# Optimization experiments

Measured on AMD Instinct MI355X. Metric: run time of the kernel, lower is better.

## Reference

```python
import jax, jax.numpy as jnp
import numpy as np

B, S, H, NH = 4, 1024, 1024, 16
HD = H // NH
CAUSAL_HEADS = 4
META_HEADS = NH // 4
CAUSAL_W = 0.7                      # cognitive_state['reasoning']['causal_active'] > 0.5 -> branch on
META_W = ((0.9 - 0.8) / 0.2) * 0.3  # awareness_level = 0.9 > 0.8 -> meta branch on, blend = 0.15


def _mha(xq, xkv, Win, bi, Wout, bout, nh):
    """torch nn.MultiheadAttention (batch_first) with packed in_proj [H, 3H]."""
    b, sq, h = xq.shape
    sk = xkv.shape[1]
    hd = h // nh
    q = (xq @ Win[:, :h] + bi[:h]).reshape(b, sq, nh, hd).transpose(0, 2, 1, 3)
    k = (xkv @ Win[:, h:2 * h] + bi[h:2 * h]).reshape(b, sk, nh, hd).transpose(0, 2, 1, 3)
    v = (xkv @ Win[:, 2 * h:] + bi[2 * h:]).reshape(b, sk, nh, hd).transpose(0, 2, 1, 3)
    scores = jnp.einsum('bhqd,bhkd->bhqk', q, k) / jnp.sqrt(jnp.asarray(hd, q.dtype))
    probs = jax.nn.softmax(scores, axis=-1)
    ctx = jnp.einsum('bhqk,bhkd->bhqd', probs, v)
    return ctx.transpose(0, 2, 1, 3).reshape(b, sq, h) @ Wout + bout


def _forward(hidden_states, cons_vec, Wq, bq, Wk, bk, Wv, bv, cg_W, cg_b, am_W, am_b,
             ca_Win, ca_bin, ca_Wout, ca_bout, mc_Win, mc_bin, mc_Wout, mc_bout, Wo, bo):
    b, s, h = hidden_states.shape
    q = (hidden_states @ Wq + bq).reshape(b, s, NH, HD).transpose(0, 2, 1, 3)
    k = (hidden_states @ Wk + bk).reshape(b, s, NH, HD).transpose(0, 2, 1, 3)
    v = (hidden_states @ Wv + bv).reshape(b, s, NH, HD).transpose(0, 2, 1, 3)
    scores = jnp.einsum('bhqd,bhkd->bhqk', q, k) / jnp.sqrt(jnp.asarray(HD, q.dtype))
    # consciousness-gated score modulation: sigmoid(gate(x) + awareness(cons_vec)) per (query, head)
    mod = jax.nn.sigmoid(hidden_states @ cg_W + cg_b + (cons_vec @ am_W + am_b))  # [B,S,NH]
    scores = scores * mod.transpose(0, 2, 1)[..., None]  # [B,NH,S,1] broadcast over keys
    probs = jax.nn.softmax(scores, axis=-1)
    ctx = jnp.einsum('bhqk,bhkd->bhqd', probs, v).transpose(0, 2, 1, 3).reshape(b, s, h)
    # causal MHA branch (active: causal_active=0.7 > 0.5)
    causal_ctx = _mha(hidden_states, hidden_states, ca_Win, ca_bin, ca_Wout, ca_bout, CAUSAL_HEADS)
    ctx = ctx * (1.0 - CAUSAL_W) + causal_ctx * CAUSAL_W
    # metacognitive MHA branch (active: awareness=0.9 > 0.8)
    meta_ctx = _mha(ctx, ctx, mc_Win, mc_bin, mc_Wout, mc_bout, META_HEADS)
    ctx = ctx * (1.0 - META_W) + meta_ctx * META_W
    return ctx @ Wo + bo


def setup_inputs() -> dict:
    key = jax.random.key(0)
    ks = jax.random.split(key, 16)
    sc = 0.02
    d = {
        'hidden_states': jax.random.normal(ks[0], (B, S, H), jnp.float32),
        'cons_vec': jax.random.uniform(ks[1], (16,), jnp.float32),
        'Wq': jax.random.normal(ks[2], (H, H), jnp.float32) * sc, 'bq': jnp.zeros((H,), jnp.float32),
        'Wk': jax.random.normal(ks[3], (H, H), jnp.float32) * sc, 'bk': jnp.zeros((H,), jnp.float32),
        'Wv': jax.random.normal(ks[4], (H, H), jnp.float32) * sc, 'bv': jnp.zeros((H,), jnp.float32),
        'cg_W': jax.random.normal(ks[5], (H, NH), jnp.float32) * sc, 'cg_b': jnp.zeros((NH,), jnp.float32),
        'am_W': jax.random.normal(ks[6], (16, NH), jnp.float32) * sc, 'am_b': jnp.zeros((NH,), jnp.float32),
        'ca_Win': jax.random.normal(ks[7], (H, 3 * H), jnp.float32) * sc, 'ca_bin': jnp.zeros((3 * H,), jnp.float32),
        'ca_Wout': jax.random.normal(ks[8], (H, H), jnp.float32) * sc, 'ca_bout': jnp.zeros((H,), jnp.float32),
        'mc_Win': jax.random.normal(ks[9], (H, 3 * H), jnp.float32) * sc, 'mc_bin': jnp.zeros((3 * H,), jnp.float32),
        'mc_Wout': jax.random.normal(ks[10], (H, H), jnp.float32) * sc, 'mc_bout': jnp.zeros((H,), jnp.float32),
        'Wo': jax.random.normal(ks[11], (H, H), jnp.float32) * sc, 'bo': jnp.zeros((H,), jnp.float32),
    }
    return d


def reference(hidden_states, cons_vec, Wq, bq, Wk, bk, Wv, bv, cg_W, cg_b, am_W, am_b,
              ca_Win, ca_bin, ca_Wout, ca_bout, mc_Win, mc_bin, mc_Wout, mc_bout, Wo, bo):
    return _forward(hidden_states, cons_vec, Wq, bq, Wk, bk, Wv, bv, cg_W, cg_b, am_W, am_b,
                    ca_Win, ca_bin, ca_Wout, ca_bout, mc_Win, mc_bin, mc_Wout, mc_bout, Wo, bo)
```

## Files before the change

### kernel.cpp

```cpp
#include <hip/hip_runtime.h>
#include <stdint.h>

typedef unsigned short u16;
typedef __attribute__((ext_vector_type(8))) short short8;
typedef __attribute__((ext_vector_type(4))) float f32x4;

#define MFMA16(a,b,c) __builtin_amdgcn_mfma_f32_16x16x32_bf16((a),(b),(c),0,0,0)

__device__ __forceinline__ u16 f2bf(float f) {
  union { float f; uint32_t u; } v; v.f = f;
  uint32_t r = v.u + 0x7FFFu + ((v.u >> 16) & 1u);
  return (u16)(r >> 16);
}
__device__ __forceinline__ float bf2f(uint32_t u) {
  union { uint32_t i; float f; } v; v.i = u << 16; return v.f;
}
__device__ __forceinline__ void async_copy16(void* lds, const void* g) {
  __builtin_amdgcn_global_load_lds(
      (const __attribute__((address_space(1))) uint32_t*)g,
      (__attribute__((address_space(3))) uint32_t*)lds, 16, 0, 0);
}

__device__ __forceinline__ void transpose8x8(uint32_t r[4], int lane8) {
  uint32_t a0, a1, a2, a3;
  a0 = __shfl_xor(r[0], 4); a1 = __shfl_xor(r[1], 4);
  a2 = __shfl_xor(r[2], 4); a3 = __shfl_xor(r[3], 4);
  if (lane8 & 4) { r[0] = a2; r[1] = a3; } else { r[2] = a0; r[3] = a1; }
  a0 = __shfl_xor(r[0], 2); a1 = __shfl_xor(r[1], 2);
  a2 = __shfl_xor(r[2], 2); a3 = __shfl_xor(r[3], 2);
  if (lane8 & 2) { r[0] = a1; r[2] = a3; } else { r[1] = a0; r[3] = a2; }
  a0 = __shfl_xor(r[0], 1); a1 = __shfl_xor(r[1], 1);
  a2 = __shfl_xor(r[2], 1); a3 = __shfl_xor(r[3], 1);
  uint32_t sel = (lane8 & 1) ? 0x03020706u : 0x05040100u;
  r[0] = __builtin_amdgcn_perm(a0, r[0], sel);
  r[1] = __builtin_amdgcn_perm(a1, r[1], sel);
  r[2] = __builtin_amdgcn_perm(a2, r[2], sel);
  r[3] = __builtin_amdgcn_perm(a3, r[3], sel);
}

__global__ __launch_bounds__(256) void castmod_kernel(
    const float* __restrict__ X, u16* __restrict__ Xbf,
    const float* __restrict__ cgW, const float* __restrict__ cgb,
    const float* __restrict__ cons, const float* __restrict__ amW,
    const float* __restrict__ amb, float* __restrict__ modp) {
  __shared__ float xs[1024];
  __shared__ float part[16][16];
  __shared__ float am[16];
  int row = blockIdx.x, t = threadIdx.x;
  {
    float4 v = ((const float4*)(X + (size_t)row * 1024))[t];
    xs[t * 4 + 0] = v.x; xs[t * 4 + 1] = v.y; xs[t * 4 + 2] = v.z; xs[t * 4 + 3] = v.w;
    uint2 o;
    o.x = (uint32_t)f2bf(v.x) | ((uint32_t)f2bf(v.y) << 16);
    o.y = (uint32_t)f2bf(v.z) | ((uint32_t)f2bf(v.w) << 16);
    ((uint2*)Xbf)[(size_t)row * 256 + t] = o;
  }
  if (t < 16) {
    float a = amb[t];
#pragma unroll
    for (int i = 0; i < 16; i++) a += cons[i] * amW[i * 16 + t];
    am[t] = a;
  }
  __syncthreads();
  int h = t & 15, ch = t >> 4;
  float p = 0.f;
#pragma unroll 8
  for (int k = ch * 64; k < ch * 64 + 64; k++) p += xs[k] * cgW[k * 16 + h];
  part[ch][h] = p;
  __syncthreads();
  if (t < 16) {
    float s = cgb[t] + am[t];
#pragma unroll
    for (int c = 0; c < 16; c++) s += part[c][t];
    int b = row >> 10, si = row & 1023;
    modp[((size_t)(b * 16 + t)) * 1024 + si] = 0.125f / (1.f + __expf(-s));
  }
}

struct PrepArgs {
  const float* src[12];
  u16* dst[12];
  int sstride[12];
  const float* cabin; const float* bq; const float* bk; const float* bv;
  float* biasBig; float* lbuf;
};
__global__ __launch_bounds__(256) void prep_weights(PrepArgs p) {
  int z = blockIdx.z;
  int tx = threadIdx.x & 31, ty = threadIdx.x >> 5;
  if (z < 12) {
    __shared__ float tile[32][33];
    const float* __restrict__ in = p.src[z];
    u16* __restrict__ out = p.dst[z];
    int sstr = p.sstride[z];
    int c0 = blockIdx.x * 32, r0 = blockIdx.y * 32;
#pragma unroll
    for (int j = 0; j < 4; j++)
      tile[ty + j * 8][tx] = in[(size_t)(r0 + ty + j * 8) * sstr + c0 + tx];
    __syncthreads();
#pragma unroll
    for (int j = 0; j < 4; j++)
      out[(size_t)(c0 + ty + j * 8) * 1024 + r0 + tx] = f2bf(tile[tx][ty + j * 8]);
  } else {
    int id = blockIdx.y * 32 + blockIdx.x, t = threadIdx.x;
    if (id < 24) {
      int i = id * 256 + t;
      float v;
      if (i < 3072) v = p.cabin[i];
      else if (i < 4096) v = p.bq[i - 3072];
      else if (i < 5120) v = p.bk[i - 4096];
      else v = p.bv[i - 5120];
      p.biasBig[i] = v;
    } else if (id < 152) {
      p.lbuf[(id - 24) * 256 + t] = 0.f;
    }
  }
}

template <int OUT_F32, int HAS_EXTRA, int BN>
__global__ __launch_bounds__(256, 3) void gemm_bt(
    const u16* __restrict__ A, const u16* __restrict__ Bt,
    const float* __restrict__ bias, const u16* __restrict__ extra,
    float alpha, float beta, void* __restrict__ Cout, int M, int N, int K) {
  constexpr int NJ = BN / 32;
  __shared__ u16 As[128 * 64];
  __shared__ u16 Bs[BN * 64];
  const int t = threadIdx.x;
  const int w = t >> 6, l = t & 63, lm = l & 15, lg = l >> 4;
  const int wm = w & 1, wn = w >> 1;
  const int m0 = blockIdx.y * 128, n0 = blockIdx.x * BN;
  const int rl = l >> 3, gsrc8 = ((l & 7) ^ (rl & 7)) * 8;
  const f32x4 fzero = {0.f, 0.f, 0.f, 0.f};
  f32x4 acc[4][NJ];
#pragma unroll
  for (int i = 0; i < 4; i++)
#pragma unroll
    for (int j = 0; j < NJ; j++) acc[i][j] = fzero;

  for (int kt = 0; kt < K; kt += 64) {
    __syncthreads();
#pragma unroll
    for (int c = 0; c < 4; c++) {
      int rb = c * 32 + w * 8;
      async_copy16(&As[rb * 64], A + (size_t)(m0 + rb + rl) * K + kt + gsrc8);
    }
#pragma unroll
    for (int c = 0; c < BN / 32; c++) {
      int rb = c * 32 + w * 8;
      async_copy16(&Bs[rb * 64], Bt + (size_t)(n0 + rb + rl) * K + kt + gsrc8);
    }
    __syncthreads();
#pragma unroll
    for (int kk = 0; kk < 2; kk++) {
      short8 af[4], bf[NJ];
      const int gph = ((kk * 4 + lg) ^ (lm & 7)) * 8;
#pragma unroll
      for (int i = 0; i < 4; i++)
        af[i] = *(const short8*)&As[(wm * 64 + i * 16 + lm) * 64 + gph];
#pragma unroll
      for (int j = 0; j < NJ; j++)
        bf[j] = *(const short8*)&Bs[(wn * (BN / 2) + j * 16 + lm) * 64 + gph];
#pragma unroll
      for (int i = 0; i < 4; i++)
#pragma unroll
        for (int j = 0; j < NJ; j++) acc[i][j] = MFMA16(af[i], bf[j], acc[i][j]);
    }
  }
#pragma unroll
  for (int i = 0; i < 4; i++) {
    int row0 = m0 + wm * 64 + i * 16 + lg * 4;
#pragma unroll
    for (int j = 0; j < NJ; j++) {
      int col = n0 + wn * (BN / 2) + j * 16 + lm;
      float bc = bias[col];
#pragma unroll
      for (int r = 0; r < 4; r++) {
        size_t idx = (size_t)(row0 + r) * N + col;
        float v = acc[i][j][r] + bc;
        if constexpr (HAS_EXTRA) v = alpha * v + beta * bf2f(extra[idx]);
        if constexpr (OUT_F32) ((float*)Cout)[idx] = v;
        else ((u16*)Cout)[idx] = f2bf(v);
      }
    }
  }
}

__global__ __launch_bounds__(256, 3) void gemm_in3(
    const u16* __restrict__ A, const u16* __restrict__ BtBig,
    const float* __restrict__ bias, u16* __restrict__ qkOut,
    u16* __restrict__ Vtb, u16* __restrict__ qkvm) {
  constexpr int K = 1024;
  __shared__ u16 As[128 * 64];
  __shared__ u16 Bs[128 * 64];
  const int t = threadIdx.x;
  const int w = t >> 6, l = t & 63, lm = l & 15, lg = l >> 4;
  const int wm = w & 1, wn = w >> 1;
  const int m0 = blockIdx.y * 128, n0 = blockIdx.x * 128;
  const int rl = l >> 3, gsrc8 = ((l & 7) ^ (rl & 7)) * 8;
  const f32x4 fzero = {0.f, 0.f, 0.f, 0.f};
  f32x4 acc[4][4];
#pragma unroll
  for (int i = 0; i < 4; i++)
#pragma unroll
    for (int j = 0; j < 4; j++) acc[i][j] = fzero;

  for (int kt = 0; kt < K; kt += 64) {
    __syncthreads();
#pragma unroll
    for (int c = 0; c < 4; c++) {
      int rb = c * 32 + w * 8;
      async_copy16(&As[rb * 64], A + (size_t)(m0 + rb + rl) * K + kt + gsrc8);
      async_copy16(&Bs[rb * 64], BtBig + (size_t)(n0 + rb + rl) * K + kt + gsrc8);
    }
    __syncthreads();
#pragma unroll
    for (int kk = 0; kk < 2; kk++) {
      short8 af[4], bf[4];
      const int gph = ((kk * 4 + lg) ^ (lm & 7)) * 8;
#pragma unroll
      for (int i = 0; i < 4; i++)
        af[i] = *(const short8*)&As[(wm * 64 + i * 16 + lm) * 64 + gph];
#pragma unroll
      for (int j = 0; j < 4; j++)
        bf[j] = *(const short8*)&Bs[(wn * 64 + j * 16 + lm) * 64 + gph];
#pragma unroll
      for (int i = 0; i < 4; i++)
#pragma unroll
        for (int j = 0; j < 4; j++) acc[i][j] = MFMA16(af[i], bf[j], acc[i][j]);
    }
  }
#pragma unroll
  for (int i = 0; i < 4; i++) {
    int row0 = m0 + wm * 64 + i * 16 + lg * 4;
#pragma unroll
    for (int j = 0; j < 4; j++) {
      int col = n0 + wn * 64 + j * 16 + lm;
      float bc = bias[col];
      if (col < 2048) {
#pragma unroll
        for (int r = 0; r < 4; r++)
          qkOut[(size_t)(row0 + r) * 2048 + col] = f2bf(acc[i][j][r] + bc);
      } else if (col < 3072) {
        int b = row0 >> 10, q0 = row0 & 1023;
        int z = b * 4 + ((col - 2048) >> 8), d = (col - 2048) & 255;
        union { u16 pk[4]; uint2 v; } u;
#pragma unroll
        for (int r = 0; r < 4; r++) u.pk[r] = f2bf(acc[i][j][r] + bc);
        *(uint2*)&Vtb[((size_t)z * 256 + d) * 1024 + q0] = u.v;
      } else {
#pragma unroll
        for (int r = 0; r < 4; r++)
          qkvm[(size_t)(row0 + r) * 3072 + col - 3072] = f2bf(acc[i][j][r] + bc);
      }
    }
  }
}

__global__ __launch_bounds__(256, 3) void gemm_qk_exp(
    const u16* __restrict__ qk, u16* __restrict__ P, float* __restrict__ lrow,
    float scale) {
  constexpr int QKS = 2048;
  __shared__ u16 As[128 * 64];
  __shared__ u16 Bs[128 * 64];
  const int t = threadIdx.x;
  const int w = t >> 6, l = t & 63, lm = l & 15, lg = l >> 4;
  const int wm = w & 1, wn = w >> 1;
  const int z = blockIdx.z, b = z >> 2, h = z & 3;
  const int m0 = blockIdx.y * 128, n0 = blockIdx.x * 128;
  const u16* Abase = qk + ((size_t)b << 10) * QKS + h * 256;
  const u16* Bbase = qk + ((size_t)b << 10) * QKS + 1024 + h * 256;
  const int rl = l >> 3, gsrc8 = ((l & 7) ^ (rl & 7)) * 8;
  const f32x4 fzero = {0.f, 0.f, 0.f, 0.f};
  f32x4 acc[4][4];
#pragma unroll
  for (int i = 0; i < 4; i++)
#pragma unroll
    for (int j = 0; j < 4; j++) acc[i][j] = fzero;

#pragma unroll
  for (int kt = 0; kt < 256; kt += 64) {
    __syncthreads();
#pragma unroll
    for (int c = 0; c < 4; c++) {
      int rb = c * 32 + w * 8;
      async_copy16(&As[rb * 64], Abase + (size_t)(m0 + rb + rl) * QKS + kt + gsrc8);
      async_copy16(&Bs[rb * 64], Bbase + (size_t)(n0 + rb + rl) * QKS + kt + gsrc8);
    }
    __syncthreads();
#pragma unroll
    for (int kk = 0; kk < 2; kk++) {
      short8 af[4], bf[4];
      const int gph = ((kk * 4 + lg) ^ (lm & 7)) * 8;
#pragma unroll
      for (int i = 0; i < 4; i++)
        af[i] = *(const short8*)&As[(wm * 64 + i * 16 + lm) * 64 + gph];
#pragma unroll
      for (int j = 0; j < 4; j++)
        bf[j] = *(const short8*)&Bs[(wn * 64 + j * 16 + lm) * 64 + gph];
#pragma unroll
      for (int i = 0; i < 4; i++)
#pragma unroll
        for (int j = 0; j < 4; j++) acc[i][j] = MFMA16(af[i], bf[j], acc[i][j]);
    }
  }
  u16* Pz = P + ((size_t)z << 20);
#pragma unroll
  for (int i = 0; i < 4; i++) {
    int row0 = m0 + wm * 64 + i * 16 + lg * 4;
    float rsum[4] = {0.f, 0.f, 0.f, 0.f};
#pragma unroll
    for (int j = 0; j < 4; j++) {
      int col = n0 + wn * 64 + j * 16 + lm;
#pragma unroll
      for (int r = 0; r < 4; r++) {
        float p = __expf(acc[i][j][r] * scale);
        rsum[r] += p;
        Pz[(size_t)(row0 + r) * 1024 + col] = f2bf(p);
      }
    }
#pragma unroll
    for (int r = 0; r < 4; r++) {
      float s = rsum[r];
#pragma unroll
      for (int sh = 1; sh <= 8; sh <<= 1) s += __shfl_xor(s, sh);
      if (lm == 0) atomicAdd(&lrow[(z << 10) + row0 + r], s);
    }
  }
}

__global__ __launch_bounds__(256, 3) void gemm_pv(
    const u16* __restrict__ P, const u16* __restrict__ Vtb,
    const float* __restrict__ lrow, u16* __restrict__ outp) {
  constexpr int K = 1024, BN = 64, NJ = 2;
  __shared__ u16 As[128 * 64];
  __shared__ u16 Bs[BN * 64];
  const int t = threadIdx.x;
  const int w = t >> 6, l = t & 63, lm = l & 15, lg = l >> 4;
  const int wm = w & 1, wn = w >> 1;
  const int z = blockIdx.z, b = z >> 2, h = z & 3;
  const int m0 = blockIdx.y * 128, n0 = blockIdx.x * BN;
  const u16* Abase = P + ((size_t)z << 20);
  const u16* Bbase = Vtb + ((size_t)z << 18);
  const int rl = l >> 3, gsrc8 = ((l & 7) ^ (rl & 7)) * 8;
  const f32x4 fzero = {0.f, 0.f, 0.f, 0.f};
  f32x4 acc[4][NJ];
#pragma unroll
  for (int i = 0; i < 4; i++)
#pragma unroll
    for (int j = 0; j < NJ; j++) acc[i][j] = fzero;

  for (int kt = 0; kt < K; kt += 64) {
    __syncthreads();
#pragma unroll
    for (int c = 0; c < 4; c++) {
      int rb = c * 32 + w * 8;
      async_copy16(&As[rb * 64], Abase + (size_t)(m0 + rb + rl) * K + kt + gsrc8);
    }
#pragma unroll
    for (int c = 0; c < BN / 32; c++) {
      int rb = c * 32 + w * 8;
      async_copy16(&Bs[rb * 64], Bbase + (size_t)(n0 + rb + rl) * K + kt + gsrc8);
    }
    __syncthreads();
#pragma unroll
    for (int kk = 0; kk < 2; kk++) {
      short8 af[4], bf[NJ];
      const int gph = ((kk * 4 + lg) ^ (lm & 7)) * 8;
#pragma unroll
      for (int i = 0; i < 4; i++)
        af[i] = *(const short8*)&As[(wm * 64 + i * 16 + lm) * 64 + gph];
#pragma unroll
      for (int j = 0; j < NJ; j++)
        bf[j] = *(const short8*)&Bs[(wn * (BN / 2) + j * 16 + lm) * 64 + gph];
#pragma unroll
      for (int i = 0; i < 4; i++)
#pragma unroll
        for (int j = 0; j < NJ; j++) acc[i][j] = MFMA16(af[i], bf[j], acc[i][j]);
    }
  }
#pragma unroll
  for (int i = 0; i < 4; i++) {
    int row0 = m0 + wm * 64 + i * 16 + lg * 4;
    float invl[4];
#pragma unroll
    for (int r = 0; r < 4; r++) invl[r] = 1.f / lrow[(z << 10) + row0 + r];
#pragma unroll
    for (int j = 0; j < NJ; j++) {
      int col = n0 + wn * (BN / 2) + j * 16 + lm;
#pragma unroll
      for (int r = 0; r < 4; r++)
        outp[(size_t)((b << 10) + row0 + r) * 1024 + h * 256 + col] =
            f2bf(acc[i][j][r] * invl[r]);
    }
  }
}

__global__ __launch_bounds__(256, 2) void flash_attn64(
    const u16* __restrict__ qkv, const float* __restrict__ modp,
    u16* __restrict__ outp) {
  constexpr int S = 1024, W3 = 3072, HD = 64, BKV = 128;
  constexpr int NKD = 2, NT = 8, ND = 4, NKP = 4, KC = 4;
  constexpr int VSTR = 136, PSTR = 136;

  __shared__ u16 Ks[BKV * HD];
  __shared__ u16 Vt[HD * VSTR];
  __shared__ u16 Ps[128 * PSTR];

  const int t = threadIdx.x, w = t >> 6, l = t & 63, lm = l & 15, lg = l >> 4;
  const int bid = blockIdx.x;
  const int rest = bid >> 3;
  const int q0 = (rest & 7) * 128;
  const int bh = (bid & 7) + 8 * (rest >> 3);
  const int b = bh >> 4, h = bh & 15;
  const size_t rowbase = (size_t)b * S;

  const int oc = t >> 3, kvo = t & 7;
  const int sd0 = (oc & 7) * 8;
  const int skvg = (oc >> 3) * 8;

  short8 qf[2][NKD];
  float rs[2][4];
#pragma unroll
  for (int qs = 0; qs < 2; qs++) {
    const u16* qp = qkv + (rowbase + q0 + qs * 64 + w * 16 + lm) * W3 + h * HD + lg * 8;
#pragma unroll
    for (int d = 0; d < NKD; d++) qf[qs][d] = *(const short8*)(qp + d * 32);
#pragma unroll
    for (int r = 0; r < 4; r++)
      rs[qs][r] = modp[(size_t)bh * S + q0 + qs * 64 + w * 16 + lg * 4 + r];
  }

  float lsum[2][4] = {{0.f, 0.f, 0.f, 0.f}, {0.f, 0.f, 0.f, 0.f}};
  const f32x4 fzero = {0.f, 0.f, 0.f, 0.f};
  f32x4 oacc[2][ND];
#pragma unroll
  for (int qs = 0; qs < 2; qs++)
#pragma unroll
    for (int d = 0; d < ND; d++) oacc[qs][d] = fzero;

  for (int kb = 0; kb < S; kb += BKV) {
    __syncthreads();
#pragma unroll
    for (int c = 0; c < 4; c++) {
      int rb = c * 32 + w * 8;
      int row = rb + (l >> 3);
      int gsrc = ((l & 7) ^ (row & 7)) * 8;
      async_copy16(&Ks[rb * HD],
                   qkv + (rowbase + kb + row) * W3 + 1024 + h * HD + gsrc);
    }
#pragma unroll
    for (int c = 0; c < KC; c++) {
      int kv = c * 32 + skvg + kvo;
      union { short8 s; uint32_t u[4]; } vv, vo;
      vv.s = *(const short8*)(qkv + (rowbase + kb + kv) * W3 + 2048 + h * HD + sd0);
      uint32_t r[4] = {vv.u[0], vv.u[1], vv.u[2], vv.u[3]};
      transpose8x8(r, kvo);
      vo.u[0] = r[0]; vo.u[1] = r[1]; vo.u[2] = r[2]; vo.u[3] = r[3];
      *(short8*)&Vt[(sd0 + kvo) * VSTR + c * 32 + skvg] = vo.s;
    }
    __syncthreads();

#pragma unroll
    for (int qs = 0; qs < 2; qs++) {
      f32x4 sacc[NT];
#pragma unroll
      for (int n = 0; n < NT; n++) sacc[n] = fzero;
#pragma unroll
      for (int n = 0; n < NT; n++) {
        int krow = n * 16 + lm;
#pragma unroll
        for (int d = 0; d < NKD; d++) {
          int g = d * 4 + lg;
          short8 kf = *(const short8*)&Ks[krow * HD + ((g ^ (krow & 7)) * 8)];
          sacc[n] = MFMA16(qf[qs][d], kf, sacc[n]);
        }
      }
#pragma unroll
      for (int n = 0; n < NT; n++) {
#pragma unroll
        for (int r = 0; r < 4; r++) {
          float p = __expf(sacc[n][r] * rs[qs][r]);
          lsum[qs][r] += p;
          Ps[(qs * 64 + w * 16 + lg * 4 + r) * PSTR + n * 16 + lm] = f2bf(p);
        }
      }
    }
#pragma unroll
    for (int qs = 0; qs < 2; qs++) {
#pragma unroll
      for (int ks = 0; ks < NKP; ks++) {
        short8 pf = *(const short8*)&Ps[(qs * 64 + w * 16 + lm) * PSTR + ks * 32 + lg * 8];
#pragma unroll
        for (int d = 0; d < ND; d++) {
          short8 vf = *(const short8*)&Vt[(d * 16 + lm) * VSTR + ks * 32 + lg * 8];
          oacc[qs][d] = MFMA16(pf, vf, oacc[qs][d]);
        }
      }
    }
  }
#pragma unroll
  for (int qs = 0; qs < 2; qs++) {
    float invl[4];
#pragma unroll
    for (int r = 0; r < 4; r++) {
      float s = lsum[qs][r];
#pragma unroll
      for (int sh = 1; sh <= 8; sh <<= 1) s += __shfl_xor(s, sh);
      invl[r] = 1.f / s;
    }
#pragma unroll
    for (int d = 0; d < ND; d++) {
      int col = h * HD + d * 16 + lm;
#pragma unroll
      for (int r = 0; r < 4; r++) {
        int row = q0 + qs * 64 + w * 16 + lg * 4 + r;
        outp[(rowbase + row) * 1024 + col] = f2bf(oacc[qs][d][r] * invl[r]);
      }
    }
  }
}

extern "C" void kernel_launch(void* const* d_in, const int* in_sizes, int n_in,
                              void* d_out, int out_size, void* d_ws, size_t ws_size,
                              hipStream_t stream) {
  (void)in_sizes; (void)n_in; (void)out_size; (void)ws_size;
  const float* X      = (const float*)d_in[0];
  const float* cons   = (const float*)d_in[1];
  const float* Wq     = (const float*)d_in[2];  const float* bq     = (const float*)d_in[3];
  const float* Wk     = (const float*)d_in[4];  const float* bk     = (const float*)d_in[5];
  const float* Wv     = (const float*)d_in[6];  const float* bv     = (const float*)d_in[7];
  const float* cgW    = (const float*)d_in[8];  const float* cgb    = (const float*)d_in[9];
  const float* amW    = (const float*)d_in[10]; const float* amb    = (const float*)d_in[11];
  const float* caWin  = (const float*)d_in[12]; const float* cabin  = (const float*)d_in[13];
  const float* caWout = (const float*)d_in[14]; const float* cabout = (const float*)d_in[15];
  const float* mcWin  = (const float*)d_in[16]; const float* mcbin  = (const float*)d_in[17];
  const float* mcWout = (const float*)d_in[18]; const float* mcbout = (const float*)d_in[19];
  const float* Wo     = (const float*)d_in[20]; const float* bo     = (const float*)d_in[21];

  char* ws = (char*)d_ws;
  size_t off = 0;
  auto alloc = [&](size_t bytes) -> void* {
    void* p = ws + off; off += (bytes + 255) & ~(size_t)255; return p;
  };
  u16*    Xbf     = (u16*)alloc((size_t)4096 * 1024 * 2);
  u16*    BtBig   = (u16*)alloc((size_t)6144 * 1024 * 2);
  u16*    mcWinT  = (u16*)alloc((size_t)3072 * 1024 * 2);
  u16*    caWoutT = (u16*)alloc((size_t)1024 * 1024 * 2);
  u16*    mcWoutT = (u16*)alloc((size_t)1024 * 1024 * 2);
  u16*    WoT     = (u16*)alloc((size_t)1024 * 1024 * 2);
  float*  biasBig = (float*)alloc(6144 * 4);
  float*  modb    = (float*)alloc((size_t)64 * 1024 * 4);
  u16*    caQK    = (u16*)alloc((size_t)4096 * 2048 * 2);
  u16*    qkvm    = (u16*)alloc((size_t)4096 * 3072 * 2);
  u16*    actx    = (u16*)alloc((size_t)4096 * 1024 * 2);
  u16*    ctxm    = (u16*)alloc((size_t)4096 * 1024 * 2);
  u16*    ctx1    = (u16*)alloc((size_t)4096 * 1024 * 2);
  u16*    Pbuf    = (u16*)alloc((size_t)16 * 1024 * 1024 * 2);
  u16*    Vtb     = (u16*)alloc((size_t)16 * 256 * 1024 * 2);
  float*  lbuf    = (float*)alloc((size_t)2 * 16384 * 4);
  float*  l_ca    = lbuf;
  float*  l_mc    = lbuf + 16384;
  u16*    mcQK    = caQK;
  u16*    mctx    = ctxm;
  u16*    ctx2    = actx;

  castmod_kernel<<<4096, 256, 0, stream>>>(X, Xbf, cgW, cgb, cons, amW, amb, modb);
  {
    PrepArgs pa;
    for (int s = 0; s < 3; s++) {
      pa.src[s] = caWin + s * 1024; pa.dst[s] = BtBig + (size_t)s * 1024 * 1024;
      pa.sstride[s] = 3072;
    }
    pa.src[3] = Wq; pa.dst[3] = BtBig + (size_t)3072 * 1024; pa.sstride[3] = 1024;
    pa.src[4] = Wk; pa.dst[4] = BtBig + (size_t)4096 * 1024; pa.sstride[4] = 1024;
    pa.src[5] = Wv; pa.dst[5] = BtBig + (size_t)5120 * 1024; pa.sstride[5] = 1024;
    for (int s = 0; s < 3; s++) {
      pa.src[6 + s] = mcWin + s * 1024; pa.dst[6 + s] = mcWinT + (size_t)s * 1024 * 1024;
      pa.sstride[6 + s] = 3072;
    }
    pa.src[9]  = caWout; pa.dst[9]  = caWoutT; pa.sstride[9]  = 1024;
    pa.src[10] = mcWout; pa.dst[10] = mcWoutT; pa.sstride[10] = 1024;
    pa.src[11] = Wo;     pa.dst[11] = WoT;     pa.sstride[11] = 1024;
    pa.cabin = cabin; pa.bq = bq; pa.bk = bk; pa.bv = bv;
    pa.biasBig = biasBig; pa.lbuf = lbuf;
    prep_weights<<<dim3(32, 32, 13), 256, 0, stream>>>(pa);
  }

  gemm_in3<<<dim3(48, 32), 256, 0, stream>>>(Xbf, BtBig, biasBig, caQK, Vtb, qkvm);
  gemm_qk_exp<<<dim3(8, 8, 16), 256, 0, stream>>>(caQK, Pbuf, l_ca, 1.f / 16.f);
  gemm_pv<<<dim3(4, 8, 16), 256, 0, stream>>>(Pbuf, Vtb, l_ca, actx);
  flash_attn64<<<512, 256, 0, stream>>>(qkvm, modb, ctxm);
  gemm_bt<0, 1, 64><<<dim3(16, 32), 256, 0, stream>>>(actx, caWoutT, cabout, ctxm, 0.7f, 0.3f,
                                                      ctx1, 4096, 1024, 1024);
  gemm_in3<<<dim3(24, 32), 256, 0, stream>>>(ctx1, mcWinT, mcbin, mcQK, Vtb, qkvm );
  gemm_qk_exp<<<dim3(8, 8, 16), 256, 0, stream>>>(mcQK, Pbuf, l_mc, 1.f / 16.f);
  gemm_pv<<<dim3(4, 8, 16), 256, 0, stream>>>(Pbuf, Vtb, l_mc, mctx);
  gemm_bt<0, 1, 64><<<dim3(16, 32), 256, 0, stream>>>(mctx, mcWoutT, mcbout, ctx1, 0.15f, 0.85f,
                                                      ctx2, 4096, 1024, 1024);
  gemm_bt<1, 0, 64><<<dim3(16, 32), 256, 0, stream>>>(ctx2, WoT, bo, nullptr, 0.f, 0.f,
                                                      d_out, 4096, 1024, 1024);
}
```

Baseline: 442.6 us.

## Fuse causal QK-exp with modulated flash attention into one launch, use 32x32 MFMA

```diff
diff --git a/kernel.cpp b/kernel.cpp
--- a/kernel.cpp
+++ b/kernel.cpp
@@ -4,8 +4,14 @@
 typedef unsigned short u16;
 typedef __attribute__((ext_vector_type(8))) short short8;
 typedef __attribute__((ext_vector_type(4))) float f32x4;
+typedef __attribute__((ext_vector_type(16))) float f32x16;
 
 #define MFMA16(a,b,c) __builtin_amdgcn_mfma_f32_16x16x32_bf16((a),(b),(c),0,0,0)
+#define MFMA32(a,b,c) __builtin_amdgcn_mfma_f32_32x32x16_bf16((a),(b),(c),0,0,0)
+
+__device__ __forceinline__ float fast_exp2(float x) {
+  return __builtin_amdgcn_exp2f(x);
+}
 
 __device__ __forceinline__ u16 f2bf(float f) {
   union { float f; uint32_t u; } v; v.f = f;
@@ -73,7 +79,7 @@
 #pragma unroll
     for (int c = 0; c < 16; c++) s += part[c][t];
     int b = row >> 10, si = row & 1023;
-    modp[((size_t)(b * 16 + t)) * 1024 + si] = 0.125f / (1.f + __expf(-s));
+    modp[((size_t)(b * 16 + t)) * 1024 + si] = 0.18033688f / (1.f + __expf(-s));
   }
 }
 
@@ -255,17 +261,17 @@
   }
 }
 
-__global__ __launch_bounds__(256, 3) void gemm_qk_exp(
-    const u16* __restrict__ qk, u16* __restrict__ P, float* __restrict__ lrow,
-    float scale) {
+__device__ __forceinline__ void qk_body(
+    char* smem, const u16* __restrict__ qk, u16* __restrict__ P,
+    float* __restrict__ lrow, float scale2, int nb, int mb, int z) {
   constexpr int QKS = 2048;
-  __shared__ u16 As[128 * 64];
-  __shared__ u16 Bs[128 * 64];
+  u16* As = (u16*)smem;
+  u16* Bs = (u16*)(smem + 128 * 64 * 2);
   const int t = threadIdx.x;
   const int w = t >> 6, l = t & 63, lm = l & 15, lg = l >> 4;
   const int wm = w & 1, wn = w >> 1;
-  const int z = blockIdx.z, b = z >> 2, h = z & 3;
-  const int m0 = blockIdx.y * 128, n0 = blockIdx.x * 128;
+  const int b = z >> 2, h = z & 3;
+  const int m0 = mb * 128, n0 = nb * 128;
   const u16* Abase = qk + ((size_t)b << 10) * QKS + h * 256;
   const u16* Bbase = qk + ((size_t)b << 10) * QKS + 1024 + h * 256;
   const int rl = l >> 3, gsrc8 = ((l & 7) ^ (rl & 7)) * 8;
@@ -312,7 +318,7 @@
       int col = n0 + wn * 64 + j * 16 + lm;
 #pragma unroll
       for (int r = 0; r < 4; r++) {
-        float p = __expf(acc[i][j][r] * scale);
+        float p = fast_exp2(acc[i][j][r] * scale2);
         rsum[r] += p;
         Pz[(size_t)(row0 + r) * 1024 + col] = f2bf(p);
       }
@@ -324,6 +330,144 @@
       for (int sh = 1; sh <= 8; sh <<= 1) s += __shfl_xor(s, sh);
       if (lm == 0) atomicAdd(&lrow[(z << 10) + row0 + r], s);
     }
+  }
+}
+
+__global__ __launch_bounds__(256, 3) void gemm_qk_exp(
+    const u16* __restrict__ qk, u16* __restrict__ P, float* __restrict__ lrow,
+    float scale2) {
+  __shared__ char smem[2 * 128 * 64 * 2];
+  qk_body(smem, qk, P, lrow, scale2, blockIdx.x, blockIdx.y, blockIdx.z);
+}
+
+__device__ __forceinline__ void flash_body(
+    char* smem, const u16* __restrict__ qkv, const float* __restrict__ modp,
+    u16* __restrict__ outp, int fid) {
+  constexpr int S = 1024, W3 = 3072, HD = 64, BKV = 128;
+  constexpr int VSTR = 136, PSTR = 136;
+  u16* Ks = (u16*)smem;
+  u16* Vt = (u16*)(smem + 16384);
+  u16* Ps = (u16*)(smem + 16384 + 17408);
+
+  const int t = threadIdx.x, w = t >> 6, l = t & 63, l31 = l & 31, hl = l >> 5;
+  const int rest = fid >> 3;
+  const int q0 = (rest & 7) * 128;
+  const int bh = (fid & 7) + 8 * (rest >> 3);
+  const int b = bh >> 4, h = bh & 15;
+  const size_t rowbase = (size_t)b * S;
+  const int qw = q0 + w * 32;
+
+  const int oc = t >> 3, kvo = t & 7;
+  const int sd0 = (oc & 7) * 8;
+  const int skvg = (oc >> 3) * 8;
+
+  short8 qf[4];
+  {
+    const u16* qp = qkv + (rowbase + qw + l31) * W3 + h * HD + hl * 8;
+#pragma unroll
+    for (int ks = 0; ks < 4; ks++) qf[ks] = *(const short8*)(qp + ks * 16);
+  }
+  float rs[16], lsum[16];
+#pragma unroll
+  for (int reg = 0; reg < 16; reg++) {
+    int qloc = (reg & 3) + 8 * (reg >> 2) + 4 * hl;
+    rs[reg] = modp[(size_t)bh * S + qw + qloc];
+    lsum[reg] = 0.f;
+  }
+  f32x16 oacc[2];
+#pragma unroll
+  for (int d = 0; d < 2; d++)
+#pragma unroll
+    for (int i = 0; i < 16; i++) oacc[d][i] = 0.f;
+
+  for (int kb = 0; kb < S; kb += BKV) {
+    __syncthreads();
+#pragma unroll
+    for (int c = 0; c < 4; c++) {
+      int rb = c * 32 + w * 8;
+      int row = rb + (l >> 3);
+      int gsrc = ((l & 7) ^ (row & 7)) * 8;
+      async_copy16(&Ks[rb * HD],
+                   qkv + (rowbase + kb + row) * W3 + 1024 + h * HD + gsrc);
+    }
+#pragma unroll
+    for (int c = 0; c < 4; c++) {
+      int kv = c * 32 + skvg + kvo;
+      union { short8 s; uint32_t u[4]; } vv, vo;
+      vv.s = *(const short8*)(qkv + (rowbase + kb + kv) * W3 + 2048 + h * HD + sd0);
+      uint32_t r[4] = {vv.u[0], vv.u[1], vv.u[2], vv.u[3]};
+      transpose8x8(r, kvo);
+      vo.u[0] = r[0]; vo.u[1] = r[1]; vo.u[2] = r[2]; vo.u[3] = r[3];
+      *(short8*)&Vt[(sd0 + kvo) * VSTR + c * 32 + skvg] = vo.s;
+    }
+    __syncthreads();
+
+    f32x16 sacc[4];
+#pragma unroll
+    for (int n = 0; n < 4; n++)
+#pragma unroll
+      for (int i = 0; i < 16; i++) sacc[n][i] = 0.f;
+#pragma unroll
+    for (int n = 0; n < 4; n++) {
+      int krow = n * 32 + l31;
+#pragma unroll
+      for (int ks = 0; ks < 4; ks++) {
+        int g = ks * 2 + hl;
+        short8 kf = *(const short8*)&Ks[krow * HD + ((g ^ (krow & 7)) * 8)];
+        sacc[n] = MFMA32(qf[ks], kf, sacc[n]);
+      }
+    }
+#pragma unroll
+    for (int n = 0; n < 4; n++) {
+#pragma unroll
+      for (int reg = 0; reg < 16; reg++) {
+        float p = fast_exp2(sacc[n][reg] * rs[reg]);
+        lsum[reg] += p;
+        int qloc = (reg & 3) + 8 * (reg >> 2) + 4 * hl;
+        Ps[(w * 32 + qloc) * PSTR + n * 32 + l31] = f2bf(p);
+      }
+    }
+#pragma unroll
+    for (int ks = 0; ks < 8; ks++) {
+      short8 pa = *(const short8*)&Ps[(w * 32 + l31) * PSTR + ks * 16 + hl * 8];
+#pragma unroll
+      for (int d = 0; d < 2; d++) {
+        short8 vb = *(const short8*)&Vt[(d * 32 + l31) * VSTR + ks * 16 + hl * 8];
+        oacc[d] = MFMA32(pa, vb, oacc[d]);
+      }
+    }
+  }
+  float invl[16];
+#pragma unroll
+  for (int reg = 0; reg < 16; reg++) {
+    float s = lsum[reg];
+#pragma unroll
+    for (int sh = 1; sh <= 16; sh <<= 1) s += __shfl_xor(s, sh);
+    invl[reg] = 1.f / s;
+  }
+#pragma unroll
+  for (int d = 0; d < 2; d++) {
+#pragma unroll
+    for (int reg = 0; reg < 16; reg++) {
+      int qloc = (reg & 3) + 8 * (reg >> 2) + 4 * hl;
+      outp[(rowbase + qw + qloc) * 1024 + h * HD + d * 32 + l31] =
+          f2bf(oacc[d][reg] * invl[reg]);
+    }
+  }
+}
+
+__global__ __launch_bounds__(256, 2) void fused_qk_flash(
+    const u16* __restrict__ qkvm, const float* __restrict__ modp,
+    u16* __restrict__ ctxm, const u16* __restrict__ caQK,
+    u16* __restrict__ P, float* __restrict__ lrow, float scale2) {
+  __shared__ char smem[16384 + 17408 + 34816];
+  const int bid = blockIdx.x;
+  const int q3 = bid / 3, m3 = bid - q3 * 3;
+  if (m3 == 2) {
+    flash_body(smem, qkvm, modp, ctxm, q3);
+  } else {
+    int qid = q3 * 2 + m3;
+    qk_body(smem, caQK, P, lrow, scale2, qid & 7, (qid >> 3) & 7, qid >> 6);
   }
 }
 
@@ -390,131 +534,6 @@
       for (int r = 0; r < 4; r++)
         outp[(size_t)((b << 10) + row0 + r) * 1024 + h * 256 + col] =
             f2bf(acc[i][j][r] * invl[r]);
-    }
-  }
-}
-
-__global__ __launch_bounds__(256, 2) void flash_attn64(
-    const u16* __restrict__ qkv, const float* __restrict__ modp,
-    u16* __restrict__ outp) {
-  constexpr int S = 1024, W3 = 3072, HD = 64, BKV = 128;
-  constexpr int NKD = 2, NT = 8, ND = 4, NKP = 4, KC = 4;
-  constexpr int VSTR = 136, PSTR = 136;
-
-  __shared__ u16 Ks[BKV * HD];
-  __shared__ u16 Vt[HD * VSTR];
-  __shared__ u16 Ps[128 * PSTR];
-
-  const int t = threadIdx.x, w = t >> 6, l = t & 63, lm = l & 15, lg = l >> 4;
-  const int bid = blockIdx.x;
-  const int rest = bid >> 3;
-  const int q0 = (rest & 7) * 128;
-  const int bh = (bid & 7) + 8 * (rest >> 3);
-  const int b = bh >> 4, h = bh & 15;
-  const size_t rowbase = (size_t)b * S;
-
-  const int oc = t >> 3, kvo = t & 7;
-  const int sd0 = (oc & 7) * 8;
-  const int skvg = (oc >> 3) * 8;
-
-  short8 qf[2][NKD];
-  float rs[2][4];
-#pragma unroll
-  for (int qs = 0; qs < 2; qs++) {
-    const u16* qp = qkv + (rowbase + q0 + qs * 64 + w * 16 + lm) * W3 + h * HD + lg * 8;
-#pragma unroll
-    for (int d = 0; d < NKD; d++) qf[qs][d] = *(const short8*)(qp + d * 32);
-#pragma unroll
-    for (int r = 0; r < 4; r++)
-      rs[qs][r] = modp[(size_t)bh * S + q0 + qs * 64 + w * 16 + lg * 4 + r];
-  }
-
-  float lsum[2][4] = {{0.f, 0.f, 0.f, 0.f}, {0.f, 0.f, 0.f, 0.f}};
-  const f32x4 fzero = {0.f, 0.f, 0.f, 0.f};
-  f32x4 oacc[2][ND];
-#pragma unroll
-  for (int qs = 0; qs < 2; qs++)
-#pragma unroll
-    for (int d = 0; d < ND; d++) oacc[qs][d] = fzero;
-
-  for (int kb = 0; kb < S; kb += BKV) {
-    __syncthreads();
-#pragma unroll
-    for (int c = 0; c < 4; c++) {
-      int rb = c * 32 + w * 8;
-      int row = rb + (l >> 3);
-      int gsrc = ((l & 7) ^ (row & 7)) * 8;
-      async_copy16(&Ks[rb * HD],
-                   qkv + (rowbase + kb + row) * W3 + 1024 + h * HD + gsrc);
-    }
-#pragma unroll
-    for (int c = 0; c < KC; c++) {
-      int kv = c * 32 + skvg + kvo;
-      union { short8 s; uint32_t u[4]; } vv, vo;
-      vv.s = *(const short8*)(qkv + (rowbase + kb + kv) * W3 + 2048 + h * HD + sd0);
-      uint32_t r[4] = {vv.u[0], vv.u[1], vv.u[2], vv.u[3]};
-      transpose8x8(r, kvo);
-      vo.u[0] = r[0]; vo.u[1] = r[1]; vo.u[2] = r[2]; vo.u[3] = r[3];
-      *(short8*)&Vt[(sd0 + kvo) * VSTR + c * 32 + skvg] = vo.s;
-    }
-    __syncthreads();
-
-#pragma unroll
-    for (int qs = 0; qs < 2; qs++) {
-      f32x4 sacc[NT];
-#pragma unroll
-      for (int n = 0; n < NT; n++) sacc[n] = fzero;
-#pragma unroll
-      for (int n = 0; n < NT; n++) {
-        int krow = n * 16 + lm;
-#pragma unroll
-        for (int d = 0; d < NKD; d++) {
-          int g = d * 4 + lg;
-          short8 kf = *(const short8*)&Ks[krow * HD + ((g ^ (krow & 7)) * 8)];
-          sacc[n] = MFMA16(qf[qs][d], kf, sacc[n]);
-        }
-      }
-#pragma unroll
-      for (int n = 0; n < NT; n++) {
-#pragma unroll
-        for (int r = 0; r < 4; r++) {
-          float p = __expf(sacc[n][r] * rs[qs][r]);
-          lsum[qs][r] += p;
-          Ps[(qs * 64 + w * 16 + lg * 4 + r) * PSTR + n * 16 + lm] = f2bf(p);
-        }
-      }
-    }
-#pragma unroll
-    for (int qs = 0; qs < 2; qs++) {
-#pragma unroll
-      for (int ks = 0; ks < NKP; ks++) {
-        short8 pf = *(const short8*)&Ps[(qs * 64 + w * 16 + lm) * PSTR + ks * 32 + lg * 8];
-#pragma unroll
-        for (int d = 0; d < ND; d++) {
-          short8 vf = *(const short8*)&Vt[(d * 16 + lm) * VSTR + ks * 32 + lg * 8];
-          oacc[qs][d] = MFMA16(pf, vf, oacc[qs][d]);
-        }
-      }
-    }
-  }
-#pragma unroll
-  for (int qs = 0; qs < 2; qs++) {
-    float invl[4];
-#pragma unroll
-    for (int r = 0; r < 4; r++) {
-      float s = lsum[qs][r];
-#pragma unroll
-      for (int sh = 1; sh <= 8; sh <<= 1) s += __shfl_xor(s, sh);
-      invl[r] = 1.f / s;
-    }
-#pragma unroll
-    for (int d = 0; d < ND; d++) {
-      int col = h * HD + d * 16 + lm;
-#pragma unroll
-      for (int r = 0; r < 4; r++) {
-        int row = q0 + qs * 64 + w * 16 + lg * 4 + r;
-        outp[(rowbase + row) * 1024 + col] = f2bf(oacc[qs][d][r] * invl[r]);
-      }
     }
   }
 }
@@ -563,6 +582,8 @@
   u16*    mctx    = ctxm;
   u16*    ctx2    = actx;
 
+  const float SC2 = 1.4426950408889634f / 16.f;
+
   castmod_kernel<<<4096, 256, 0, stream>>>(X, Xbf, cgW, cgb, cons, amW, amb, modb);
   {
     PrepArgs pa;
@@ -586,13 +607,12 @@
   }
 
   gemm_in3<<<dim3(48, 32), 256, 0, stream>>>(Xbf, BtBig, biasBig, caQK, Vtb, qkvm);
-  gemm_qk_exp<<<dim3(8, 8, 16), 256, 0, stream>>>(caQK, Pbuf, l_ca, 1.f / 16.f);
+  fused_qk_flash<<<1536, 256, 0, stream>>>(qkvm, modb, ctxm, caQK, Pbuf, l_ca, SC2);
   gemm_pv<<<dim3(4, 8, 16), 256, 0, stream>>>(Pbuf, Vtb, l_ca, actx);
-  flash_attn64<<<512, 256, 0, stream>>>(qkvm, modb, ctxm);
   gemm_bt<0, 1, 64><<<dim3(16, 32), 256, 0, stream>>>(actx, caWoutT, cabout, ctxm, 0.7f, 0.3f,
                                                       ctx1, 4096, 1024, 1024);
   gemm_in3<<<dim3(24, 32), 256, 0, stream>>>(ctx1, mcWinT, mcbin, mcQK, Vtb, qkvm );
-  gemm_qk_exp<<<dim3(8, 8, 16), 256, 0, stream>>>(mcQK, Pbuf, l_mc, 1.f / 16.f);
+  gemm_qk_exp<<<dim3(8, 8, 16), 256, 0, stream>>>(mcQK, Pbuf, l_mc, SC2);
   gemm_pv<<<dim3(4, 8, 16), 256, 0, stream>>>(Pbuf, Vtb, l_mc, mctx);
   gemm_bt<0, 1, 64><<<dim3(16, 32), 256, 0, stream>>>(mctx, mcWoutT, mcbout, ctx1, 0.15f, 0.85f,
                                                       ctx2, 4096, 1024, 1024);
```

Result: faster. 432.4 us (-2.3%).
